# Optimization experiments

Hardware: AMD Instinct MI355X
Metric: run time of the kernel (lower is better)

## Reference

```python
import jax, jax.numpy as jnp
import numpy as np

B, T, DM = 2, 512, 1024
H, DH = 16, 64          # n_heads, d_head = d_model // n_heads
D, R = 32, 4            # d_manifold, metric_net rank
TEMP_MIN = 0.5


def _rope_tables(t_len, d_head):
    inv_freq = 1.0 / (10000.0 ** (jnp.arange(0, d_head, 2, dtype=jnp.float32) / d_head))
    t = jnp.arange(t_len, dtype=jnp.float32)
    freqs = t[:, None] * inv_freq[None, :]          # [T, d_head//2]
    emb = jnp.concatenate([freqs, freqs], axis=-1)  # [T, d_head]
    return jnp.cos(emb), jnp.sin(emb)


def _apply_rope(x, cos, sin):
    # x: [B, H, T, d_head]
    half = x.shape[-1] // 2
    x1, x2 = x[..., :half], x[..., half:]
    c1 = cos[None, None, :, :half]
    s1 = sin[None, None, :, :half]
    return jnp.concatenate([x1 * c1 - x2 * s1, x1 * s1 + x2 * c1], axis=-1)


def setup_inputs() -> dict:
    key = jax.random.key(0)
    ks = jax.random.split(key, 9)
    s = 0.02
    return {
        "x": jax.random.normal(ks[0], (B, T, DM), dtype=jnp.float32),
        "Wq": s * jax.random.normal(ks[1], (DM, DM), dtype=jnp.float32),
        "Wk": s * jax.random.normal(ks[2], (DM, DM), dtype=jnp.float32),
        "Wv": s * jax.random.normal(ks[3], (DM, DM), dtype=jnp.float32),
        "Wo": s * jax.random.normal(ks[4], (DM, DM), dtype=jnp.float32),
        "Wqm": s * jax.random.normal(ks[5], (DH, D), dtype=jnp.float32),
        "Wkm": s * jax.random.normal(ks[6], (DH, D), dtype=jnp.float32),
        "Wmetric": s * jax.random.normal(ks[7], (D, D * R), dtype=jnp.float32),
        "temperature": jnp.asarray(1.0, dtype=jnp.float32),
    }


def reference(x, Wq, Wk, Wv, Wo, Wqm, Wkm, Wmetric, temperature):
    b, t, c = x.shape
    # projections -> [B, H, T, d_head]
    def split_heads(y):
        return y.reshape(b, t, H, DH).transpose(0, 2, 1, 3)
    q = split_heads(x @ Wq)
    k = split_heads(x @ Wk)
    v = split_heads(x @ Wv)

    cos, sin = _rope_tables(t, DH)
    q = _apply_rope(q, cos, sin)
    k = _apply_rope(k, cos, sin)

    # manifold coordinates in (0,1): [B, H, T, D]
    qm = jax.nn.sigmoid(jnp.einsum('bhtd,dm->bhtm', q, Wqm))
    km = jax.nn.sigmoid(jnp.einsum('bhtd,dm->bhtm', k, Wkm))

    # low-rank metric factor U(q): [B, H, T, D, R]
    U = jnp.einsum('bhtm,mn->bhtn', qm, Wmetric).reshape(b, H, t, D, R)

    # Euclidean part: ||q_i - k_j||^2 = |q|^2 + |k|^2 - 2 q.k  -> [B,H,T,T]
    q2 = jnp.sum(qm * qm, axis=-1)
    k2 = jnp.sum(km * km, axis=-1)
    qk = jnp.einsum('bhid,bhjd->bhij', qm, km)
    dist_euc = q2[..., :, None] + k2[..., None, :] - 2.0 * qk

    # low-rank part: ||U_i^T (q_i - k_j)||^2, factorized as U_i^T q_i - U_i^T k_j
    Uq = jnp.einsum('bhidr,bhid->bhir', U, qm)          # [B,H,T,R]
    Uk = jnp.einsum('bhidr,bhjd->bhijr', U, km)         # [B,H,T,T,R]
    dist_lr = jnp.sum((Uq[:, :, :, None, :] - Uk) ** 2, axis=-1)

    dist_sq = jnp.maximum(dist_euc + dist_lr, 0.0)

    temp = jnp.maximum(temperature, TEMP_MIN)
    attn = -dist_sq / temp

    causal = jnp.triu(jnp.ones((t, t), dtype=bool), k=1)
    attn = jnp.where(causal[None, None], -jnp.inf, attn)
    attn = jax.nn.softmax(attn, axis=-1)

    out = jnp.einsum('bhij,bhjd->bhid', attn, v)        # [B,H,T,d_head]
    out = out.transpose(0, 2, 1, 3).reshape(b, t, c)
    return out @ Wo
```

## Files before the change

### kernel.cpp

```cpp
#include <hip/hip_runtime.h>
#include <cmath>

constexpr int B_  = 2;
constexpr int T_  = 512;
constexpr int DM_ = 1024;
constexpr int H_  = 16;
constexpr int DH_ = 64;
constexpr int D_  = 32;
constexpr int R_  = 4;
constexpr int BH_ = B_ * H_;

typedef __bf16 bf16x8 __attribute__((ext_vector_type(8)));
typedef float  f32x4  __attribute__((ext_vector_type(4)));
typedef unsigned short u16x8 __attribute__((ext_vector_type(8)));

__device__ __forceinline__ unsigned short f2bf(float f) {
    unsigned u = __float_as_uint(f);
    return (unsigned short)((u + 0x7fffu + ((u >> 16) & 1u)) >> 16);
}
__device__ __forceinline__ float bf2f(unsigned short v) {
    return __uint_as_float((unsigned)v << 16);
}
__device__ __forceinline__ void gload16(const void* g, void* l) {
    __builtin_amdgcn_global_load_lds(
        (const __attribute__((address_space(1))) void*)g,
        (__attribute__((address_space(3))) void*)l, 16, 0, 0);
}

__global__ __launch_bounds__(256) void prep_kernel(
    const float* __restrict__ x,
    const float* __restrict__ Wq, const float* __restrict__ Wk,
    const float* __restrict__ Wv, const float* __restrict__ Wo,
    unsigned short* __restrict__ xb,
    unsigned short* __restrict__ wqb, unsigned short* __restrict__ wkb,
    unsigned short* __restrict__ wvb, unsigned short* __restrict__ wob)
{
    const int t = threadIdx.x;
    const int z = blockIdx.z;
    if (z == 4) {
        int base = (blockIdx.y * 16 + blockIdx.x) * 4096 + t * 16;
#pragma unroll
        for (int c = 0; c < 4; ++c) {
            float4 v = *(const float4*)&x[base + c * 4];
            ushort4 o = { f2bf(v.x), f2bf(v.y), f2bf(v.z), f2bf(v.w) };
            *(ushort4*)&xb[base + c * 4] = o;
        }
        return;
    }
    __shared__ __align__(16) unsigned short Ls[64][72];
    const float* W = (z == 0) ? Wq : (z == 1) ? Wk : (z == 2) ? Wv : Wo;
    unsigned short* O = (z == 0) ? wqb : (z == 1) ? wkb : (z == 2) ? wvb : wob;
    const int k0 = blockIdx.x * 64;
    const int n0 = blockIdx.y * 64;
#pragma unroll
    for (int it = 0; it < 4; ++it) {
        int r = it * 16 + (t >> 4);
        int c = (t & 15) * 4;
        float4 v4 = *(const float4*)&W[(size_t)(k0 + r) * DM_ + n0 + c];
        Ls[c + 0][r] = f2bf(v4.x); Ls[c + 1][r] = f2bf(v4.y);
        Ls[c + 2][r] = f2bf(v4.z); Ls[c + 3][r] = f2bf(v4.w);
    }
    __syncthreads();
#pragma unroll
    for (int it = 0; it < 2; ++it) {
        int nl = it * 32 + (t >> 3);
        int kc = (t & 7) * 8;
        *(u16x8*)&O[(size_t)(n0 + nl) * DM_ + k0 + kc] = *(const u16x8*)&Ls[nl][kc];
    }
}

__global__ __launch_bounds__(256) void gemm_qkv(
    const unsigned short* __restrict__ A,
    const unsigned short* __restrict__ Bt0,
    const unsigned short* __restrict__ Bt1,
    const unsigned short* __restrict__ Bt2,
    float* __restrict__ C0, float* __restrict__ C1,
    unsigned short* __restrict__ vT)
{
    __shared__ __align__(16) unsigned short As[2][2][64 * 64];
    __shared__ __align__(16) unsigned short Bs[2][2][64 * 64];
    const int tid  = threadIdx.x;
    const int lane = tid & 63;
    const int w    = tid >> 6;
    const int wm   = (w & 1) * 32;
    const int wn   = (w >> 1) * 32;
    const int l15  = lane & 15, quad = lane >> 4;

    const int bm = blockIdx.y * 64;
    const int n0 = blockIdx.x * 64;
    const int which = n0 >> 10;
    const int bn = n0 & 1023;
    const unsigned short* Bt = (which == 0) ? Bt0 : (which == 1) ? Bt1 : Bt2;

    const int srow = tid >> 3, kcs = tid & 7, kcg = kcs ^ (srow & 7);
    const unsigned short* Ap0 = A  + (size_t)(bm + srow) * DM_ + kcg * 8;
    const unsigned short* Bp0 = Bt + (size_t)(bn + srow) * DM_ + kcg * 8;
    const unsigned short* Ap1 = Ap0 + 32 * DM_;
    const unsigned short* Bp1 = Bp0 + 32 * DM_;

#pragma unroll
    for (int hf = 0; hf < 2; ++hf) {
        gload16(Ap0 + hf * 64, &As[0][hf][tid * 8]);
        gload16(Ap1 + hf * 64, &As[0][hf][tid * 8 + 2048]);
        gload16(Bp0 + hf * 64, &Bs[0][hf][tid * 8]);
        gload16(Bp1 + hf * 64, &Bs[0][hf][tid * 8 + 2048]);
    }

    f32x4 acc[2][2] = {};
#pragma unroll
    for (int k = 0; k < 8; ++k) {
        const int cur = k & 1, nxt = cur ^ 1;
        __builtin_amdgcn_s_barrier();
        if (k + 1 < 8) {
            const int off = (k + 1) * 128;
#pragma unroll
            for (int hf = 0; hf < 2; ++hf) {
                gload16(Ap0 + off + hf * 64, &As[nxt][hf][tid * 8]);
                gload16(Ap1 + off + hf * 64, &As[nxt][hf][tid * 8 + 2048]);
                gload16(Bp0 + off + hf * 64, &Bs[nxt][hf][tid * 8]);
                gload16(Bp1 + off + hf * 64, &Bs[nxt][hf][tid * 8 + 2048]);
            }
            __builtin_amdgcn_s_waitcnt(0x0F78);
        } else {
            __builtin_amdgcn_s_waitcnt(0x0F70);
        }
        __builtin_amdgcn_s_barrier();

#pragma unroll
        for (int hf = 0; hf < 2; ++hf) {
            bf16x8 af[2][2], bfr[2][2];
#pragma unroll
            for (int ki = 0; ki < 2; ++ki)
#pragma unroll
                for (int i = 0; i < 2; ++i) {
                    int ra = wm + i * 16 + l15;
                    int rb = wn + i * 16 + l15;
                    int kch = ki * 4 + quad;
                    af[ki][i]  = *(const bf16x8*)&As[cur][hf][ra * 64 + (kch ^ (ra & 7)) * 8];
                    bfr[ki][i] = *(const bf16x8*)&Bs[cur][hf][rb * 64 + (kch ^ (rb & 7)) * 8];
                }
#pragma unroll
            for (int mi = 0; mi < 2; ++mi)
#pragma unroll
                for (int ni = 0; ni < 2; ++ni) {
                    acc[mi][ni] = __builtin_amdgcn_mfma_f32_16x16x32_bf16(
                        af[0][mi], bfr[0][ni], acc[mi][ni], 0, 0, 0);
                    acc[mi][ni] = __builtin_amdgcn_mfma_f32_16x16x32_bf16(
                        af[1][mi], bfr[1][ni], acc[mi][ni], 0, 0, 0);
                }
        }
    }

#pragma unroll
    for (int mi = 0; mi < 2; ++mi)
#pragma unroll
        for (int ni = 0; ni < 2; ++ni) {
            f32x4 a = acc[mi][ni];
            int col = wn + ni * 16 + l15;
            int h = bn >> 6, d = col;
#pragma unroll
            for (int r = 0; r < 4; ++r) {
                int row = bm + wm + mi * 16 + quad * 4 + r;
                int bb = row >> 9, tt = row & (T_ - 1);
                if (which == 2) {
                    vT[(((size_t)bb * H_ + h) * DH_ + d) * T_ + tt] = f2bf(a[r]);
                } else {
                    float* C = (which == 0) ? C0 : C1;
                    C[(((size_t)bb * H_ + h) * T_ + tt) * DH_ + d] = a[r];
                }
            }
        }
}

__global__ __launch_bounds__(256) void gemm_out(
    const unsigned short* __restrict__ A,
    const unsigned short* __restrict__ Bt,
    float* __restrict__ C0)
{
    __shared__ __align__(16) unsigned short As[3][64 * 64];
    __shared__ __align__(16) unsigned short Bs[3][64 * 64];
    const int tid  = threadIdx.x;
    const int lane = tid & 63;
    const int w    = tid >> 6;
    const int wm   = (w & 1) * 32;
    const int wn   = (w >> 1) * 32;
    const int l15  = lane & 15, quad = lane >> 4;

    const int bm = blockIdx.y * 64;
    const int bn = blockIdx.x * 64;

    const int srow = tid >> 3, kcs = tid & 7, kcg = kcs ^ (srow & 7);
    const unsigned short* Ap0 = A  + (size_t)(bm + srow) * DM_ + kcg * 8;
    const unsigned short* Bp0 = Bt + (size_t)(bn + srow) * DM_ + kcg * 8;
    const unsigned short* Ap1 = Ap0 + 32 * DM_;
    const unsigned short* Bp1 = Bp0 + 32 * DM_;

    gload16(Ap0, &As[0][tid * 8]);
    gload16(Ap1, &As[0][tid * 8 + 2048]);
    gload16(Bp0, &Bs[0][tid * 8]);
    gload16(Bp1, &Bs[0][tid * 8 + 2048]);
    gload16(Ap0 + 64, &As[1][tid * 8]);
    gload16(Ap1 + 64, &As[1][tid * 8 + 2048]);
    gload16(Bp0 + 64, &Bs[1][tid * 8]);
    gload16(Bp1 + 64, &Bs[1][tid * 8 + 2048]);

    f32x4 acc[2][2] = {};
#pragma unroll
    for (int k = 0; k < 16; ++k) {
        const int cur = k % 3, pre = (k + 2) % 3;
        __builtin_amdgcn_s_barrier();
        if (k + 2 < 16) {
            const int off = (k + 2) * 64;
            gload16(Ap0 + off, &As[pre][tid * 8]);
            gload16(Ap1 + off, &As[pre][tid * 8 + 2048]);
            gload16(Bp0 + off, &Bs[pre][tid * 8]);
            gload16(Bp1 + off, &Bs[pre][tid * 8 + 2048]);
            __builtin_amdgcn_s_waitcnt(0x0F78);
        } else if (k + 1 < 16) {
            __builtin_amdgcn_s_waitcnt(0x0F74);
        } else {
            __builtin_amdgcn_s_waitcnt(0x0F70);
        }
        __builtin_amdgcn_s_barrier();

        bf16x8 af[2][2], bfr[2][2];
#pragma unroll
        for (int ki = 0; ki < 2; ++ki)
#pragma unroll
            for (int i = 0; i < 2; ++i) {
                int ra = wm + i * 16 + l15;
                int rb = wn + i * 16 + l15;
                int kch = ki * 4 + quad;
                af[ki][i]  = *(const bf16x8*)&As[cur][ra * 64 + (kch ^ (ra & 7)) * 8];
                bfr[ki][i] = *(const bf16x8*)&Bs[cur][rb * 64 + (kch ^ (rb & 7)) * 8];
            }
#pragma unroll
        for (int mi = 0; mi < 2; ++mi)
#pragma unroll
            for (int ni = 0; ni < 2; ++ni) {
                acc[mi][ni] = __builtin_amdgcn_mfma_f32_16x16x32_bf16(
                    af[0][mi], bfr[0][ni], acc[mi][ni], 0, 0, 0);
                acc[mi][ni] = __builtin_amdgcn_mfma_f32_16x16x32_bf16(
                    af[1][mi], bfr[1][ni], acc[mi][ni], 0, 0, 0);
            }
    }

#pragma unroll
    for (int mi = 0; mi < 2; ++mi)
#pragma unroll
        for (int ni = 0; ni < 2; ++ni) {
            f32x4 a = acc[mi][ni];
            int col = wn + ni * 16 + l15;
#pragma unroll
            for (int r = 0; r < 4; ++r) {
                int row = bm + wm + mi * 16 + quad * 4 + r;
                C0[(size_t)row * DM_ + bn + col] = a[r];
            }
        }
}

__global__ __launch_bounds__(256) void feat_both(
    const float* __restrict__ q_raw, const float* __restrict__ k_raw,
    const float* __restrict__ Wqm,   const float* __restrict__ Wkm,
    const float* __restrict__ Wmetric,
    unsigned short* __restrict__ a_hi, unsigned short* __restrict__ a_lo,
    unsigned short* __restrict__ km_hi, unsigned short* __restrict__ km_lo,
    float* __restrict__ q2p, float* __restrict__ k2,
    unsigned short* __restrict__ Urb)
{
    const bool QSIDE = (blockIdx.y == 0);
    const float* raw = QSIDE ? q_raw : k_raw;
    const float* Wm  = QSIDE ? Wqm   : Wkm;

    __shared__ float qrs[4][64];
    __shared__ float qms[4][32];
    const int tid  = threadIdx.x;
    const int w    = tid >> 6;
    const int lane = tid & 63;
    const int row  = blockIdx.x * 4 + w;
    const int t    = row & (T_ - 1);
    const int bh   = row >> 9;

    const int m  = lane & 31;
    const int hh = lane >> 5;

    float rv = raw[(size_t)row * 64 + lane];
    float ang = (float)t * expf((float)m * -0.28782313662425575f);
    float s, c;
    sincosf(ang, &s, &c);
    float partner = __shfl_xor(rv, 32);
    float qr = (lane < 32) ? (rv * c - partner * s) : (partner * s + rv * c);
    qrs[w][lane] = qr;

    float acc = 0.f;
#pragma unroll 8
    for (int i = 0; i < 32; ++i) {
        int d = hh * 32 + i;
        acc += qrs[w][d] * Wm[d * 32 + m];
    }
    acc += __shfl_xor(acc, 32);
    const float qm = 1.0f / (1.0f + __expf(-acc));
    if (hh == 0) qms[w][m] = qm;

    if (!QSIDE) {
        if (lane < 32) {
            unsigned short hi = f2bf(qm);
            unsigned short lo = f2bf(qm - bf2f(hi));
            size_t off = (size_t)row * 32 + lane;
            km_hi[off] = hi; km_lo[off] = lo;
        }
        float sq = (lane < 32) ? qm * qm : 0.f;
        sq += __shfl_xor(sq, 32); sq += __shfl_xor(sq, 16);
        sq += __shfl_xor(sq, 8);  sq += __shfl_xor(sq, 4);
        sq += __shfl_xor(sq, 2);  sq += __shfl_xor(sq, 1);
        if (lane == 0) k2[row] = sq;
        return;
    }

    float a0 = 0.f, a1 = 0.f;
#pragma unroll 8
    for (int mm = 0; mm < 32; ++mm) {
        float qv = qms[w][mm];
        float2 wv = *(const float2*)&Wmetric[mm * 128 + lane * 2];
        a0 += qv * wv.x;
        a1 += qv * wv.y;
    }

    {
        int n0i = lane * 2;
        int r0 = n0i & 3, d0 = n0i >> 2;
        Urb[(((size_t)bh * R_ + r0    ) * T_ + t) * D_ + d0] = f2bf(a0);
        Urb[(((size_t)bh * R_ + r0 + 1) * T_ + t) * D_ + d0] = f2bf(a1);
    }

    float dq = qms[w][lane >> 1];
    float u0 = a0 * dq, u1 = a1 * dq;
    u0 += __shfl_xor(u0, 2);  u1 += __shfl_xor(u1, 2);
    u0 += __shfl_xor(u0, 4);  u1 += __shfl_xor(u1, 4);
    u0 += __shfl_xor(u0, 8);  u1 += __shfl_xor(u1, 8);
    u0 += __shfl_xor(u0, 16); u1 += __shfl_xor(u1, 16);
    u0 += __shfl_xor(u0, 32); u1 += __shfl_xor(u1, 32);
    float v0 = __shfl_xor(u0, 1), v1 = __shfl_xor(u1, 1);
    const bool odd = (lane & 1);
    float Uq0 = odd ? v0 : u0;
    float Uq1 = odd ? v1 : u1;
    float Uq2 = odd ? u0 : v0;
    float Uq3 = odd ? u1 : v1;

    {
        int src = m * 2;
        float s0 = __shfl(a0, src);
        float s1 = __shfl(a1, src);
        float s2 = __shfl(a0, src + 1);
        float s3 = __shfl(a1, src + 1);
        if (lane < 32) {
            float b = Uq0 * s0 + Uq1 * s1 + Uq2 * s2 + Uq3 * s3;
            float a = qm + b;
            unsigned short hi = f2bf(a);
            unsigned short lo = f2bf(a - bf2f(hi));
            size_t off = (size_t)row * 32 + lane;
            a_hi[off] = hi; a_lo[off] = lo;
        }
    }

    float sq = (lane < 32) ? qm * qm : 0.f;
    sq += __shfl_xor(sq, 32); sq += __shfl_xor(sq, 16);
    sq += __shfl_xor(sq, 8);  sq += __shfl_xor(sq, 4);
    sq += __shfl_xor(sq, 2);  sq += __shfl_xor(sq, 1);
    if (lane == 0)
        q2p[row] = sq + Uq0 * Uq0 + Uq1 * Uq1 + Uq2 * Uq2 + Uq3 * Uq3;
}

constexpr int PROW = 40;
__global__ __launch_bounds__(256) void attn_mfma(
    const unsigned short* __restrict__ a_hi, const unsigned short* __restrict__ a_lo,
    const unsigned short* __restrict__ km_hi, const unsigned short* __restrict__ km_lo,
    const unsigned short* __restrict__ Urb,
    const float* __restrict__ q2p, const float* __restrict__ k2,
    const float* __restrict__ temp_p, const unsigned short* __restrict__ vT,
    unsigned short* __restrict__ ctxb)
{
    __shared__ __align__(16) unsigned short P_lds[4][32 * PROW];
    __shared__ __align__(16) float OP[4][32][64];
    __shared__ float ML[4][32];

    const int itile = blockIdx.x, bh = blockIdx.y;
    const int i0 = itile * 32;
    const int tid = threadIdx.x, w = tid >> 6, lane = tid & 63;
    const int l15 = lane & 15, quad = lane >> 4;

    const float inv_temp = 1.0f / fmaxf(temp_p[0], 0.5f);

    bf16x8 Ahi[2], Alo[2], Aur[4][2];
#pragma unroll
    for (int mi = 0; mi < 2; ++mi) {
        size_t ab = ((size_t)bh * T_ + i0 + mi * 16 + l15) * 32 + quad * 8;
        Ahi[mi] = *(const bf16x8*)&a_hi[ab];
        Alo[mi] = *(const bf16x8*)&a_lo[ab];
#pragma unroll
        for (int r = 0; r < 4; ++r)
            Aur[r][mi] = *(const bf16x8*)
                &Urb[(((size_t)bh * R_ + r) * T_ + i0 + mi * 16 + l15) * 32 + quad * 8];
    }
    float q2r[2][4];
#pragma unroll
    for (int mi = 0; mi < 2; ++mi)
#pragma unroll
        for (int rg = 0; rg < 4; ++rg)
            q2r[mi][rg] = q2p[(size_t)bh * T_ + i0 + mi * 16 + quad * 4 + rg];

    f32x4 Oacc[2][4] = {};
    float psum[2][4] = {};

    for (int jt = w; jt <= itile; jt += 4) {
        const int j0 = jt * 32;
        bf16x8 Bhi[2], Blo[2];
#pragma unroll
        for (int ni = 0; ni < 2; ++ni) {
            size_t kb = ((size_t)bh * T_ + j0 + ni * 16 + l15) * 32 + quad * 8;
            Bhi[ni] = *(const bf16x8*)&km_hi[kb];
            Blo[ni] = *(const bf16x8*)&km_lo[kb];
        }
        f32x4 acc[2][2] = {};
#pragma unroll
        for (int mi = 0; mi < 2; ++mi)
#pragma unroll
            for (int ni = 0; ni < 2; ++ni) {
                acc[mi][ni] = __builtin_amdgcn_mfma_f32_16x16x32_bf16(
                    Alo[mi], Bhi[ni], acc[mi][ni], 0, 0, 0);
                acc[mi][ni] = __builtin_amdgcn_mfma_f32_16x16x32_bf16(
                    Ahi[mi], Blo[ni], acc[mi][ni], 0, 0, 0);
                acc[mi][ni] = __builtin_amdgcn_mfma_f32_16x16x32_bf16(
                    Ahi[mi], Bhi[ni], acc[mi][ni], 0, 0, 0);
            }
        f32x4 sq[2][2] = {};
#pragma unroll
        for (int r = 0; r < 4; ++r) {
            f32x4 ar[2][2] = {};
#pragma unroll
            for (int mi = 0; mi < 2; ++mi)
#pragma unroll
                for (int ni = 0; ni < 2; ++ni)
                    ar[mi][ni] = __builtin_amdgcn_mfma_f32_16x16x32_bf16(
                        Aur[r][mi], Bhi[ni], ar[mi][ni], 0, 0, 0);
#pragma unroll
            for (int mi = 0; mi < 2; ++mi)
#pragma unroll
                for (int ni = 0; ni < 2; ++ni)
                    sq[mi][ni] += ar[mi][ni] * ar[mi][ni];
        }
        float k2c[2];
#pragma unroll
        for (int ni = 0; ni < 2; ++ni)
            k2c[ni] = k2[(size_t)bh * T_ + j0 + ni * 16 + l15];
        const bool diag = (jt == itile);
#pragma unroll
        for (int mi = 0; mi < 2; ++mi)
#pragma unroll
            for (int ni = 0; ni < 2; ++ni)
#pragma unroll
                for (int rg = 0; rg < 4; ++rg) {
                    float dist = q2r[mi][rg] + k2c[ni]
                               - 2.f * acc[mi][ni][rg] + sq[mi][ni][rg];
                    float sc = -fmaxf(dist, 0.f) * inv_temp;
                    if (diag && (ni * 16 + l15) > (mi * 16 + quad * 4 + rg))
                        sc = -1e30f;
                    float p = __expf(sc);
                    psum[mi][rg] += p;
                    P_lds[w][(mi * 16 + quad * 4 + rg) * PROW + ni * 16 + l15] = f2bf(p);
                }
        bf16x8 Pf[2], Vf[4];
#pragma unroll
        for (int mi = 0; mi < 2; ++mi)
            Pf[mi] = *(const bf16x8*)&P_lds[w][(mi * 16 + l15) * PROW + quad * 8];
#pragma unroll
        for (int n4 = 0; n4 < 4; ++n4)
            Vf[n4] = *(const bf16x8*)
                &vT[((size_t)bh * DH_ + n4 * 16 + l15) * T_ + j0 + quad * 8];
#pragma unroll
        for (int mi = 0; mi < 2; ++mi)
#pragma unroll
            for (int n4 = 0; n4 < 4; ++n4)
                Oacc[mi][n4] = __builtin_amdgcn_mfma_f32_16x16x32_bf16(
                    Pf[mi], Vf[n4], Oacc[mi][n4], 0, 0, 0);
    }

#pragma unroll
    for (int mi = 0; mi < 2; ++mi)
#pragma unroll
        for (int rg = 0; rg < 4; ++rg) {
            float v = psum[mi][rg];
            v += __shfl_xor(v, 1); v += __shfl_xor(v, 2);
            v += __shfl_xor(v, 4); v += __shfl_xor(v, 8);
            psum[mi][rg] = v;
        }
    if (l15 == 0)
#pragma unroll
        for (int mi = 0; mi < 2; ++mi)
#pragma unroll
            for (int rg = 0; rg < 4; ++rg)
                ML[w][mi * 16 + quad * 4 + rg] = psum[mi][rg];
#pragma unroll
    for (int mi = 0; mi < 2; ++mi)
#pragma unroll
        for (int n4 = 0; n4 < 4; ++n4)
#pragma unroll
            for (int rg = 0; rg < 4; ++rg)
                OP[w][mi * 16 + quad * 4 + rg][n4 * 16 + l15] = Oacc[mi][n4][rg];
    __syncthreads();

    const int ii = tid >> 3, ds = tid & 7;
    float l = ML[0][ii] + ML[1][ii] + ML[2][ii] + ML[3][ii];
    float O[8] = {};
#pragma unroll
    for (int wv = 0; wv < 4; ++wv) {
        float4 o0 = *(const float4*)&OP[wv][ii][ds * 8];
        float4 o1 = *(const float4*)&OP[wv][ii][ds * 8 + 4];
        O[0] += o0.x; O[1] += o0.y; O[2] += o0.z; O[3] += o0.w;
        O[4] += o1.x; O[5] += o1.y; O[6] += o1.z; O[7] += o1.w;
    }
    const float inv = 1.0f / l;
    const int b = bh >> 4, h = bh & 15;
    u16x8 o;
#pragma unroll
    for (int dd = 0; dd < 8; ++dd) o[dd] = f2bf(O[dd] * inv);
    *(u16x8*)&ctxb[((size_t)b * T_ + i0 + ii) * DM_ + h * 64 + ds * 8] = o;
}

extern "C" void kernel_launch(void* const* d_in, const int* in_sizes, int n_in,
                              void* d_out, int out_size, void* d_ws, size_t ws_size,
                              hipStream_t stream)
{
    const float* x       = (const float*)d_in[0];
    const float* Wq      = (const float*)d_in[1];
    const float* Wk      = (const float*)d_in[2];
    const float* Wv      = (const float*)d_in[3];
    const float* Wo      = (const float*)d_in[4];
    const float* Wqm     = (const float*)d_in[5];
    const float* Wkm     = (const float*)d_in[6];
    const float* Wmetric = (const float*)d_in[7];
    const float* temp    = (const float*)d_in[8];
    float* out = (float*)d_out;
    float* ws  = (float*)d_ws;

    float* q_raw = ws;
    float* k_raw = q_raw + (size_t)BH_ * T_ * DH_;
    float* q2p   = k_raw + (size_t)BH_ * T_ * DH_;
    float* k2    = q2p   + (size_t)BH_ * T_;
    unsigned short* xb   = (unsigned short*)(k2 + (size_t)BH_ * T_);
    unsigned short* wqb  = xb   + (size_t)DM_ * DM_;
    unsigned short* wkb  = wqb  + (size_t)DM_ * DM_;
    unsigned short* wvb  = wkb  + (size_t)DM_ * DM_;
    unsigned short* wob  = wvb  + (size_t)DM_ * DM_;
    unsigned short* a_hi = wob  + (size_t)DM_ * DM_;
    unsigned short* a_lo = a_hi + (size_t)BH_ * T_ * D_;
    unsigned short* kmhi = a_lo + (size_t)BH_ * T_ * D_;
    unsigned short* kmlo = kmhi + (size_t)BH_ * T_ * D_;
    unsigned short* Urb  = kmlo + (size_t)BH_ * T_ * D_;
    unsigned short* vT   = Urb  + (size_t)BH_ * R_ * T_ * D_;
    unsigned short* ctxb = (unsigned short*)q_raw;

    prep_kernel<<<dim3(16, 16, 5), 256, 0, stream>>>(
        x, Wq, Wk, Wv, Wo, xb, wqb, wkb, wvb, wob);
    gemm_qkv<<<dim3(48, 16), 256, 0, stream>>>(
        xb, wqb, wkb, wvb, q_raw, k_raw, vT);
    feat_both<<<dim3(BH_ * T_ / 4, 2), 256, 0, stream>>>(
        q_raw, k_raw, Wqm, Wkm, Wmetric,
        a_hi, a_lo, kmhi, kmlo, q2p, k2, Urb);
    attn_mfma<<<dim3(T_ / 32, BH_), 256, 0, stream>>>(
        a_hi, a_lo, kmhi, kmlo, Urb, q2p, k2, temp, vT, ctxb);
    gemm_out<<<dim3(16, 16), 256, 0, stream>>>(
        ctxb, wob, out);
}
```

Baseline: 150.3 us.

## Load QKV GEMM B-operand fragments directly into registers, stage only A in LDS

The QKV projection GEMM now stages only the A tile through LDS. Each wave reads its own 16-column slice of the weight matrix straight from global memory into registers, prefetching one k-step ahead. The k-step shrinks from 128 to 64 and the warp layout changes to 4 waves by 16 columns, each wave computing four 16x16 tiles. This removes the LDS traffic and space for B, which should raise occupancy and cut LDS reads. In exchange there are twice as many barrier iterations, and the uncoalesced per-lane global loads of B depend on the wait count covering register loads correctly.

After: 150.3 us. No clear change (+0.0%).

```diff
diff --git a/kernel.cpp b/kernel.cpp
--- a/kernel.cpp
+++ b/kernel.cpp
@@ -77,13 +77,11 @@
     float* __restrict__ C0, float* __restrict__ C1,
     unsigned short* __restrict__ vT)
 {
-    __shared__ __align__(16) unsigned short As[2][2][64 * 64];
-    __shared__ __align__(16) unsigned short Bs[2][2][64 * 64];
+    __shared__ __align__(16) unsigned short As[2][64 * 64];
     const int tid  = threadIdx.x;
     const int lane = tid & 63;
     const int w    = tid >> 6;
-    const int wm   = (w & 1) * 32;
-    const int wn   = (w >> 1) * 32;
+    const int wn   = w * 16;
     const int l15  = lane & 15, quad = lane >> 4;
 
     const int bm = blockIdx.y * 64;
@@ -93,83 +91,68 @@
     const unsigned short* Bt = (which == 0) ? Bt0 : (which == 1) ? Bt1 : Bt2;
 
     const int srow = tid >> 3, kcs = tid & 7, kcg = kcs ^ (srow & 7);
-    const unsigned short* Ap0 = A  + (size_t)(bm + srow) * DM_ + kcg * 8;
-    const unsigned short* Bp0 = Bt + (size_t)(bn + srow) * DM_ + kcg * 8;
+    const unsigned short* Ap0 = A + (size_t)(bm + srow) * DM_ + kcg * 8;
     const unsigned short* Ap1 = Ap0 + 32 * DM_;
-    const unsigned short* Bp1 = Bp0 + 32 * DM_;
-
-#pragma unroll
-    for (int hf = 0; hf < 2; ++hf) {
-        gload16(Ap0 + hf * 64, &As[0][hf][tid * 8]);
-        gload16(Ap1 + hf * 64, &As[0][hf][tid * 8 + 2048]);
-        gload16(Bp0 + hf * 64, &Bs[0][hf][tid * 8]);
-        gload16(Bp1 + hf * 64, &Bs[0][hf][tid * 8 + 2048]);
-    }
-
-    f32x4 acc[2][2] = {};
-#pragma unroll
-    for (int k = 0; k < 8; ++k) {
+    const unsigned short* Bp  = Bt + (size_t)(bn + wn + l15) * DM_ + quad * 8;
+
+    gload16(Ap0, &As[0][tid * 8]);
+    gload16(Ap1, &As[0][tid * 8 + 2048]);
+    bf16x8 bcur[2];
+    bcur[0] = *(const bf16x8*)&Bp[0];
+    bcur[1] = *(const bf16x8*)&Bp[32];
+
+    f32x4 acc[4] = {};
+#pragma unroll
+    for (int k = 0; k < 16; ++k) {
         const int cur = k & 1, nxt = cur ^ 1;
         __builtin_amdgcn_s_barrier();
-        if (k + 1 < 8) {
-            const int off = (k + 1) * 128;
-#pragma unroll
-            for (int hf = 0; hf < 2; ++hf) {
-                gload16(Ap0 + off + hf * 64, &As[nxt][hf][tid * 8]);
-                gload16(Ap1 + off + hf * 64, &As[nxt][hf][tid * 8 + 2048]);
-                gload16(Bp0 + off + hf * 64, &Bs[nxt][hf][tid * 8]);
-                gload16(Bp1 + off + hf * 64, &Bs[nxt][hf][tid * 8 + 2048]);
-            }
-            __builtin_amdgcn_s_waitcnt(0x0F78);
+        bf16x8 bnxt[2];
+        if (k + 1 < 16) {
+            const int off = (k + 1) * 64;
+            gload16(Ap0 + off, &As[nxt][tid * 8]);
+            gload16(Ap1 + off, &As[nxt][tid * 8 + 2048]);
+            bnxt[0] = *(const bf16x8*)&Bp[off];
+            bnxt[1] = *(const bf16x8*)&Bp[off + 32];
+            __builtin_amdgcn_s_waitcnt(0x0F74);
         } else {
             __builtin_amdgcn_s_waitcnt(0x0F70);
         }
         __builtin_amdgcn_s_barrier();
 
 #pragma unroll
-        for (int hf = 0; hf < 2; ++hf) {
-            bf16x8 af[2][2], bfr[2][2];
-#pragma unroll
-            for (int ki = 0; ki < 2; ++ki)
-#pragma unroll
-                for (int i = 0; i < 2; ++i) {
-                    int ra = wm + i * 16 + l15;
-                    int rb = wn + i * 16 + l15;
-                    int kch = ki * 4 + quad;
-                    af[ki][i]  = *(const bf16x8*)&As[cur][hf][ra * 64 + (kch ^ (ra & 7)) * 8];
-                    bfr[ki][i] = *(const bf16x8*)&Bs[cur][hf][rb * 64 + (kch ^ (rb & 7)) * 8];
-                }
-#pragma unroll
-            for (int mi = 0; mi < 2; ++mi)
-#pragma unroll
-                for (int ni = 0; ni < 2; ++ni) {
-                    acc[mi][ni] = __builtin_amdgcn_mfma_f32_16x16x32_bf16(
-                        af[0][mi], bfr[0][ni], acc[mi][ni], 0, 0, 0);
-                    acc[mi][ni] = __builtin_amdgcn_mfma_f32_16x16x32_bf16(
-                        af[1][mi], bfr[1][ni], acc[mi][ni], 0, 0, 0);
-                }
-        }
-    }
-
-#pragma unroll
-    for (int mi = 0; mi < 2; ++mi)
-#pragma unroll
-        for (int ni = 0; ni < 2; ++ni) {
-            f32x4 a = acc[mi][ni];
-            int col = wn + ni * 16 + l15;
-            int h = bn >> 6, d = col;
-#pragma unroll
-            for (int r = 0; r < 4; ++r) {
-                int row = bm + wm + mi * 16 + quad * 4 + r;
-                int bb = row >> 9, tt = row & (T_ - 1);
-                if (which == 2) {
-                    vT[(((size_t)bb * H_ + h) * DH_ + d) * T_ + tt] = f2bf(a[r]);
-                } else {
-                    float* C = (which == 0) ? C0 : C1;
-                    C[(((size_t)bb * H_ + h) * T_ + tt) * DH_ + d] = a[r];
-                }
+        for (int ki = 0; ki < 2; ++ki) {
+            const int kch = ki * 4 + quad;
+            bf16x8 af[4];
+#pragma unroll
+            for (int mi = 0; mi < 4; ++mi) {
+                int ra = mi * 16 + l15;
+                af[mi] = *(const bf16x8*)&As[cur][ra * 64 + (kch ^ (ra & 7)) * 8];
             }
-        }
+#pragma unroll
+            for (int mi = 0; mi < 4; ++mi)
+                acc[mi] = __builtin_amdgcn_mfma_f32_16x16x32_bf16(
+                    af[mi], bcur[ki], acc[mi], 0, 0, 0);
+        }
+        if (k + 1 < 16) { bcur[0] = bnxt[0]; bcur[1] = bnxt[1]; }
+    }
+
+#pragma unroll
+    for (int mi = 0; mi < 4; ++mi) {
+        f32x4 a = acc[mi];
+        int col = wn + l15;
+        int h = bn >> 6, d = col;
+#pragma unroll
+        for (int r = 0; r < 4; ++r) {
+            int row = bm + mi * 16 + quad * 4 + r;
+            int bb = row >> 9, tt = row & (T_ - 1);
+            if (which == 2) {
+                vT[(((size_t)bb * H_ + h) * DH_ + d) * T_ + tt] = f2bf(a[r]);
+            } else {
+                float* C = (which == 0) ? C0 : C1;
+                C[(((size_t)bb * H_ + h) * T_ + tt) * DH_ + d] = a[r];
+            }
+        }
+    }
 }
 
 __global__ __launch_bounds__(256) void gemm_out(
```
